# Kernel tuning notes

Measured on AMD Instinct MI355X. Metric: run time of the kernel, lower is better.

Reference implementation:

```python
import jax, jax.numpy as jnp
import numpy as np

HID, NQ, NKV, HD = 4096, 32, 8, 128
EPS = 1e-6
GOLDEN = 1.618033988749895
BASE = 10000.0


def _rmsnorm(x, w, eps=EPS):
    var = jnp.mean(x.astype(jnp.float32) ** 2, axis=-1, keepdims=True)
    return (x * jax.lax.rsqrt(var + eps)).astype(x.dtype) * w


def _rope_half(t, pos, inv_freq):
    # t: (B,T,H,dh); pos: (B,T); inv_freq: (dh//2,)
    ang = pos.astype(jnp.float32)[..., None] * inv_freq  # (B,T,dq)
    cos = jnp.cos(ang)[:, :, None, :]
    sin = jnp.sin(ang)[:, :, None, :]
    dq = inv_freq.shape[0]
    t1, t2 = t[..., :dq], t[..., dq:]
    return jnp.concatenate([t1 * cos - t2 * sin, t1 * sin + t2 * cos], axis=-1)


def _apply_ggrope(q, k, row_ids, col_ids):
    # 2D RoPE: first half of head_dim encodes rows, second half encodes cols;
    # column frequencies scaled by the golden ratio (GGRoPE).
    dh = HD // 2
    inv_freq = 1.0 / (BASE ** (jnp.arange(0, dh, 2, dtype=jnp.float32) / dh))
    inv_freq_col = inv_freq * GOLDEN

    def rot(t):
        tr = _rope_half(t[..., :dh], row_ids, inv_freq)
        tc = _rope_half(t[..., dh:], col_ids, inv_freq_col)
        return jnp.concatenate([tr, tc], axis=-1)

    return rot(q), rot(k)


def setup_inputs() -> dict:
    key = jax.random.key(0)
    ks = jax.random.split(key, 9)
    B, T = 1, 2048
    s = 0.02
    return {
        "x": jax.random.normal(ks[0], (B, T, HID), jnp.float32),
        "row_ids": jax.random.randint(ks[1], (B, T), 0, 30),
        "col_ids": jax.random.randint(ks[2], (B, T), 0, 30),
        "attention_mask": jnp.zeros((B, 1, T, T), jnp.float32),
        "Wq": jax.random.normal(ks[3], (HID, NQ * HD), jnp.float32) * s,
        "Wk": jax.random.normal(ks[4], (HID, NKV * HD), jnp.float32) * s,
        "Wv": jax.random.normal(ks[5], (HID, NKV * HD), jnp.float32) * s,
        "Wo": jax.random.normal(ks[6], (NQ * HD, HID), jnp.float32) * s,
        "q_norm_w": jnp.ones((HD,), jnp.float32),
        "k_norm_w": jnp.ones((HD,), jnp.float32),
    }


def reference(x, row_ids, col_ids, attention_mask, Wq, Wk, Wv, Wo, q_norm_w, k_norm_w):
    B, T, _ = x.shape
    group = NQ // NKV
    q = (x @ Wq).reshape(B, T, NQ, HD)
    k = (x @ Wk).reshape(B, T, NKV, HD)
    v = (x @ Wv).reshape(B, T, NKV, HD)
    q = _rmsnorm(q, q_norm_w)
    k = _rmsnorm(k, k_norm_w)
    q, k = _apply_ggrope(q, k, row_ids, col_ids)
    # expand KV heads to match query heads (GQA)
    k = jnp.repeat(k, group, axis=2)  # (B,T,NQ,HD)
    v = jnp.repeat(v, group, axis=2)
    q = q.transpose(0, 2, 1, 3)  # (B,NQ,T,HD)
    k = k.transpose(0, 2, 1, 3)
    v = v.transpose(0, 2, 1, 3)
    ssmax_scale = (HD ** -0.5) * np.log(max(T, 2)).astype(np.float32)
    scores = jnp.einsum("bhqd,bhkd->bhqk", q, k) * ssmax_scale
    scores = scores + attention_mask
    attn = jax.nn.softmax(scores.astype(jnp.float32), axis=-1).astype(q.dtype)
    out = jnp.einsum("bhqk,bhkd->bhqd", attn, v)
    out = out.transpose(0, 2, 1, 3).reshape(B, T, NQ * HD)
    return out @ Wo
```

## Files before the change

kernel.cpp:

```cpp
#include <hip/hip_runtime.h>
#include <hip/hip_bf16.h>

typedef unsigned short u16;
typedef __attribute__((ext_vector_type(8))) short bf16x8;
typedef __attribute__((ext_vector_type(4))) float f32x4;

#define LOG2E_F 1.4426950408889634f
#define QSCALE (0.08838834764831845f * 7.625595228825695f * 1.4426950408889634f)

__device__ __forceinline__ u16 f2bf(float f) {
  unsigned x = __float_as_uint(f);
  unsigned r = (x + 0x7fffu + ((x >> 16) & 1u)) >> 16;
  return (u16)r;
}
__device__ __forceinline__ float bf2f(u16 u) {
  return __uint_as_float(((unsigned)u) << 16);
}
__device__ __forceinline__ float exp2a(float x) {
  float r;
  asm("v_exp_f32 %0, %1" : "=v"(r) : "v"(x));
  return r;
}
__device__ __forceinline__ unsigned cvtpk(float lo, float hi) {
  unsigned r;
  asm("v_cvt_pk_bf16_f32 %0, %1, %2" : "=v"(r) : "v"(lo), "v"(hi));
  return r;
}

__device__ __forceinline__ void gload_lds16(const void* g, void* l) {
  __builtin_amdgcn_global_load_lds(
      (__attribute__((address_space(1))) void*)(g),
      (__attribute__((address_space(3))) void*)(l), 16, 0, 0);
}

__device__ __forceinline__ f32x4 mfma16(bf16x8 a, bf16x8 b, f32x4 c) {
  return __builtin_amdgcn_mfma_f32_16x16x32_bf16(a, b, c, 0, 0, 0);
}

__global__ __launch_bounds__(256) void cvt_x(const float4* __restrict__ x,
                                             ushort4* __restrict__ xb) {
  size_t i = (size_t)blockIdx.x * 256 + threadIdx.x;
  float4 v = x[i];
  ushort4 o;
  o.x = f2bf(v.x); o.y = f2bf(v.y); o.z = f2bf(v.z); o.w = f2bf(v.w);
  xb[i] = o;
}

__global__ __launch_bounds__(256) void tcvt(const float* __restrict__ src,
                                            u16* __restrict__ dst, int N) {
  __shared__ float t[64][65];
  int bid = blockIdx.x;
  int kt = bid & 63, nt = bid >> 6;
  int k0 = kt * 64, n0 = nt * 64;
  int tid = threadIdx.x;
#pragma unroll
  for (int it = 0; it < 16; ++it) {
    int idx = it * 256 + tid;
    int row = idx >> 6, col = idx & 63;
    t[row][col] = src[(size_t)(k0 + row) * N + n0 + col];
  }
  __syncthreads();
#pragma unroll
  for (int it = 0; it < 8; ++it) {
    int idx = it * 256 + tid;
    int nrow = idx >> 5, kc = idx & 31;
    ushort2 o;
    o.x = f2bf(t[kc * 2][nrow]);
    o.y = f2bf(t[kc * 2 + 1][nrow]);
    *(ushort2*)&dst[(size_t)(n0 + nrow) * 4096 + k0 + kc * 2] = o;
  }
}

__global__ __launch_bounds__(256) void maskflag(const float4* __restrict__ mask,
                                                int* __restrict__ flag) {
  size_t i = (size_t)blockIdx.x * 256 + threadIdx.x;
  float4 v = mask[i];
  if (v.x != 0.f || v.y != 0.f || v.z != 0.f || v.w != 0.f) atomicOr(flag, 1);
}

__global__ __launch_bounds__(256) void trig_kernel(const int* __restrict__ row_ids,
                                                   const int* __restrict__ col_ids,
                                                   float4* __restrict__ trig) {
  int idx = blockIdx.x * 256 + threadIdx.x;
  int tok = idx >> 5, i = idx & 31;
  float inv = exp2f(-(float)i * 0.41524101186092030f);
  float ar = (float)row_ids[tok] * inv;
  float ac = (float)col_ids[tok] * inv * 1.618033988749895f;
  float4 o;
  o.x = cosf(ar); o.y = sinf(ar); o.z = cosf(ac); o.w = sinf(ac);
  trig[idx] = o;
}

__global__ __launch_bounds__(256) void rope_kernel(u16* __restrict__ qk,
                                                   const float4* __restrict__ trig,
                                                   const float* __restrict__ qw,
                                                   const float* __restrict__ kw) {
  const int tok = blockIdx.x;
  const int tid = threadIdx.x;
  const int w = tid >> 6, lane = tid & 63;
  float4 t4 = trig[tok * 32 + (lane & 31)];
  float sgn = (lane < 32) ? -1.0f : 1.0f;

  for (int it = 0; it < 10; ++it) {
    int hh = w + it * 4;
    bool isQ = (hh < 32);
    int colbase = isQ ? hh * 128 : 4096 + (hh - 32) * 128;
    const float* nw = isQ ? qw : kw;
    float scale = isQ ? QSCALE : 1.0f;
    u16* p = qk + (size_t)tok * 5120 + colbase;
    float v1 = bf2f(p[lane]);
    float v2 = bf2f(p[64 + lane]);
    float w1 = nw[lane], w2 = nw[64 + lane];
    float ss = v1 * v1 + v2 * v2;
    ss += __shfl_xor(ss, 1);  ss += __shfl_xor(ss, 2);  ss += __shfl_xor(ss, 4);
    ss += __shfl_xor(ss, 8);  ss += __shfl_xor(ss, 16); ss += __shfl_xor(ss, 32);
    float rinv = rsqrtf(ss * (1.0f / 128.0f) + 1e-6f);
    float n1 = v1 * rinv * w1;
    float n2 = v2 * rinv * w2;
    float p1 = __shfl_xor(n1, 32);
    float p2 = __shfl_xor(n2, 32);
    float r1 = n1 * t4.x + sgn * p1 * t4.y;
    float r2 = n2 * t4.z + sgn * p2 * t4.w;
    p[lane]      = f2bf(r1 * scale);
    p[64 + lane] = f2bf(r2 * scale);
  }
}

template <int MODE>
__global__ __launch_bounds__(512, 2) void gemm256(const u16* __restrict__ A,
                                                  const u16* __restrict__ Bt,
                                                  void* __restrict__ C0,
                                                  u16* __restrict__ Vt, int nnt) {
  extern __shared__ char smem[];
  const int tid = threadIdx.x, lane = tid & 63, w = tid >> 6;
  const int l15 = lane & 15, l4 = lane >> 4;
  const int wr = w >> 2, wc = w & 3;

  const int grid = gridDim.x;
  const int wgid = (blockIdx.x & 7) * (grid >> 3) + (blockIdx.x >> 3);
  const int mt = wgid / nnt, nt = wgid % nnt;
  const int m0 = mt * 256, n0 = nt * 256;

  const int kswz = (((tid & 7) ^ ((tid >> 3) & 7)) << 4);
  const char* arow = (const char*)A + (size_t)(m0 + (tid >> 3)) * 8192 + kswz;
  const char* brow = (const char*)Bt + (size_t)(n0 + (tid >> 3)) * 8192 + kswz;

  auto stageA = [&](int t, int h) {
#pragma unroll
    for (int rd = 0; rd < 2; ++rd)
      gload_lds16(arow + (size_t)(h * 128 + rd * 64) * 8192 + t * 128,
                  smem + ((t & 1) * 2 + h) * 16384 + rd * 8192 + w * 1024);
  };
  auto stageB = [&](int t, int h) {
#pragma unroll
    for (int rd = 0; rd < 2; ++rd)
      gload_lds16(brow + (size_t)(h * 128 + rd * 64) * 8192 + t * 128,
                  smem + 65536 + ((t & 1) * 2 + h) * 16384 + rd * 8192 + w * 1024);
  };

  f32x4 acc[8][4];
#pragma unroll
  for (int i = 0; i < 8; ++i)
#pragma unroll
    for (int j = 0; j < 4; ++j) acc[i][j] = (f32x4){0.f, 0.f, 0.f, 0.f};

  const int aoff0 = ((l4) ^ (l15 & 7)) << 4;
  const int aoff1 = ((4 + l4) ^ (l15 & 7)) << 4;

  stageA(0, 0); stageA(0, 1);
  stageB(0, 0); stageB(0, 1);
  stageB(1, 0); stageB(1, 1);
  asm volatile("s_waitcnt vmcnt(4)" ::: "memory");
  __builtin_amdgcn_s_barrier();

  auto do_iter = [&](int t0, int last) {
    bf16x8 bfr[4][2];
#pragma unroll
    for (int p = 0; p < 8; ++p) {
      const int s = p >> 2, qd = p & 3;
      const char* aT = smem + (s * 2 + wr) * 16384 + l15 * 128;
      bf16x8 afr[2][2];
#pragma unroll
      for (int jm = 0; jm < 2; ++jm) {
        afr[jm][0] = *(const bf16x8*)(aT + (2 * qd + jm) * 2048 + aoff0);
        afr[jm][1] = *(const bf16x8*)(aT + (2 * qd + jm) * 2048 + aoff1);
      }
      if (qd == 0) {
        const char* bT = smem + 65536 + (s * 2 + (wc >> 1)) * 16384 +
                         ((wc & 1) * 64 + l15) * 128;
#pragma unroll
        for (int nf = 0; nf < 4; ++nf) {
          bfr[nf][0] = *(const bf16x8*)(bT + nf * 2048 + aoff0);
          bfr[nf][1] = *(const bf16x8*)(bT + nf * 2048 + aoff1);
        }
      }
      if (p == 0) { stageA(t0 + 1, 0); stageA(t0 + 1, 1); }
      if (!last) {
        if (p == 1) stageB(t0 + 2, 0);
        if (p == 2) stageB(t0 + 2, 1);
        if (p == 4) { stageA(t0 + 2, 0); stageA(t0 + 2, 1); }
        if (p == 5) stageB(t0 + 3, 0);
        if (p == 6) stageB(t0 + 3, 1);
      }
      if (p == 3) {
        if (last) asm volatile("s_waitcnt vmcnt(0)" ::: "memory");
        else      asm volatile("s_waitcnt vmcnt(4)" ::: "memory");
      }
      if (p == 7 && !last) asm volatile("s_waitcnt vmcnt(4)" ::: "memory");
      __builtin_amdgcn_s_barrier();
      asm volatile("s_waitcnt lgkmcnt(0)" ::: "memory");
      __builtin_amdgcn_sched_barrier(0);
      __builtin_amdgcn_s_setprio(1);
#pragma unroll
      for (int ks = 0; ks < 2; ++ks)
#pragma unroll
        for (int jm = 0; jm < 2; ++jm)
#pragma unroll
          for (int nf = 0; nf < 4; ++nf)
            acc[2 * qd + jm][nf] =
                mfma16(afr[jm][ks], bfr[nf][ks], acc[2 * qd + jm][nf]);
      __builtin_amdgcn_s_setprio(0);
      __builtin_amdgcn_s_barrier();
    }
  };

  for (int j = 0; j < 31; ++j) do_iter(2 * j, 0);
  do_iter(62, 1);

  if (MODE == 0) {
    if (n0 < 5120) {
      u16* qkp = (u16*)C0;
#pragma unroll
      for (int mf = 0; mf < 8; ++mf)
#pragma unroll
        for (int nf = 0; nf < 4; ++nf) {
          int ng = n0 + wc * 64 + nf * 16 + l15;
#pragma unroll
          for (int r = 0; r < 4; ++r) {
            int mg = m0 + wr * 128 + mf * 16 + l4 * 4 + r;
            qkp[(size_t)mg * 5120 + ng] = f2bf(acc[mf][nf][r]);
          }
        }
    } else {
#pragma unroll
      for (int mf = 0; mf < 8; ++mf)
#pragma unroll
        for (int nf = 0; nf < 4; ++nf) {
          int vr = (n0 - 5120) + wc * 64 + nf * 16 + l15;
          int mg = m0 + wr * 128 + mf * 16 + l4 * 4;
          ushort4 pk;
          pk.x = f2bf(acc[mf][nf][0]); pk.y = f2bf(acc[mf][nf][1]);
          pk.z = f2bf(acc[mf][nf][2]); pk.w = f2bf(acc[mf][nf][3]);
          *(ushort4*)&Vt[(size_t)vr * 2048 + mg] = pk;
        }
    }
  } else {
    float* Cp = (float*)C0;
#pragma unroll
    for (int mf = 0; mf < 8; ++mf)
#pragma unroll
      for (int nf = 0; nf < 4; ++nf) {
        int ng = n0 + wc * 64 + nf * 16 + l15;
#pragma unroll
        for (int r = 0; r < 4; ++r) {
          int mg = m0 + wr * 128 + mf * 16 + l4 * 4 + r;
          Cp[(size_t)mg * 4096 + ng] = acc[mf][nf][r];
        }
      }
  }
}

__global__ __launch_bounds__(512, 2) void attn_kernel(const u16* __restrict__ qk,
                                                      const u16* __restrict__ vt,
                                                      u16* __restrict__ oat,
                                                      const float* __restrict__ mask,
                                                      const int* __restrict__ flag) {
  __shared__ u16 k_lds[2][64 * 128];
  __shared__ u16 v_lds[2][64 * 128];

  const int tid = threadIdx.x, lane = tid & 63, w = tid >> 6;
  const int l15 = lane & 15, l4 = lane >> 4;
  const int bid = blockIdx.x;
  const int hk = bid & 7;
  const int rest = bid >> 3;
  const int h = hk * 4 + (rest & 3);
  const int qt = rest >> 2;
  const int qbase = qt * 256 + w * 32;

  const bool use_mask = (*flag != 0);
  const char* kbase = (const char*)qk + 8192 + (size_t)hk * 256;
  const char* vbase = (const char*)vt + (size_t)hk * 128 * 4096;

  bf16x8 qf[2][4];
#pragma unroll
  for (int qg = 0; qg < 2; ++qg) {
    const char* qp = (const char*)qk +
                     (size_t)(qbase + qg * 16 + l15) * 10240 + h * 256 + l4 * 16;
#pragma unroll
    for (int ks = 0; ks < 4; ++ks) qf[qg][ks] = *(const bf16x8*)(qp + ks * 64);
  }

  f32x4 oacc[2][8];
#pragma unroll
  for (int qg = 0; qg < 2; ++qg)
#pragma unroll
    for (int fd = 0; fd < 8; ++fd) oacc[qg][fd] = (f32x4){0.f, 0.f, 0.f, 0.f};
  float m_run[2] = {-1e30f, -1e30f};
  float l_run[2] = {0.f, 0.f};

  int koff[4], voff[2];
#pragma unroll
  for (int ks = 0; ks < 4; ++ks) koff[ks] = ((4 * ks + l4) ^ l15) << 4;
#pragma unroll
  for (int ks = 0; ks < 2; ++ks) voff[ks] = ((4 * ks + l4) ^ (l15 & 7)) << 4;

#define STAGE(buf, kv0)                                                        \
  {                                                                            \
    _Pragma("unroll") for (int rd = 0; rd < 2; ++rd) {                         \
      int c = rd * 512 + tid;                                                  \
      int row = c >> 4;                                                        \
      int src = ((c & 15) ^ (row & 15)) << 4;                                  \
      gload_lds16(kbase + (size_t)((kv0) + row) * 10240 + src,                 \
                  (char*)k_lds[buf] + (rd * 512 + w * 64) * 16);               \
      int rowv = c >> 3;                                                       \
      int srcv = ((c & 7) ^ (rowv & 7)) << 4;                                  \
      gload_lds16(vbase + (size_t)rowv * 4096 + (kv0) * 2 + srcv,              \
                  (char*)v_lds[buf] + (rd * 512 + w * 64) * 16);               \
    }                                                                          \
  }

  STAGE(0, 0);
  asm volatile("s_waitcnt vmcnt(0)" ::: "memory");
  __builtin_amdgcn_s_barrier();
  __builtin_amdgcn_sched_barrier(0);

  for (int kt = 0; kt < 32; ++kt) {
    const int cur = kt & 1;
    const int kv0 = kt * 64;
    if (kt < 31) STAGE(cur ^ 1, kv0 + 64);

    f32x4 sA[2][4];
#pragma unroll
    for (int qg = 0; qg < 2; ++qg)
#pragma unroll
      for (int f = 0; f < 4; ++f) sA[qg][f] = (f32x4){0.f, 0.f, 0.f, 0.f};

    __builtin_amdgcn_s_setprio(1);
#pragma unroll
    for (int ks = 0; ks < 4; ++ks) {
      bf16x8 kfr[4];
#pragma unroll
      for (int f = 0; f < 4; ++f)
        kfr[f] = *(const bf16x8*)((const char*)k_lds[cur] +
                                  (16 * f + l15) * 256 + koff[ks]);
#pragma unroll
      for (int f = 0; f < 4; ++f) {
        sA[0][f] = mfma16(kfr[f], qf[0][ks], sA[0][f]);
        sA[1][f] = mfma16(kfr[f], qf[1][ks], sA[1][f]);
      }
    }
    __builtin_amdgcn_s_setprio(0);

    if (use_mask) {
#pragma unroll
      for (int qg = 0; qg < 2; ++qg) {
        int qglob = qbase + qg * 16 + l15;
#pragma unroll
        for (int f = 0; f < 4; ++f)
#pragma unroll
          for (int r = 0; r < 4; ++r) {
            int kvglob = kv0 + 16 * f + 4 * l4 + r;
            sA[qg][f][r] += LOG2E_F * mask[(size_t)qglob * 2048 + kvglob];
          }
      }
    }

    unsigned paw[2][2][4];
#pragma unroll
    for (int qg = 0; qg < 2; ++qg) {
      float mx = fmaxf(fmaxf(fmaxf(sA[qg][0][0], sA[qg][0][1]),
                             fmaxf(sA[qg][0][2], sA[qg][0][3])),
                       fmaxf(fmaxf(sA[qg][1][0], sA[qg][1][1]),
                             fmaxf(sA[qg][1][2], sA[qg][1][3])));
      float mx2 = fmaxf(fmaxf(fmaxf(sA[qg][2][0], sA[qg][2][1]),
                              fmaxf(sA[qg][2][2], sA[qg][2][3])),
                        fmaxf(fmaxf(sA[qg][3][0], sA[qg][3][1]),
                              fmaxf(sA[qg][3][2], sA[qg][3][3])));
      mx = fmaxf(mx, mx2);
      mx = fmaxf(mx, __shfl_xor(mx, 16));
      mx = fmaxf(mx, __shfl_xor(mx, 32));
      if (__any(mx > m_run[qg] + 8.0f)) {
        float mnew = fmaxf(m_run[qg], mx);
        float a = exp2a(m_run[qg] - mnew);
        l_run[qg] *= a;
        m_run[qg] = mnew;
        float a0 = __shfl(a, 4 * l4 + 0);
        float a1 = __shfl(a, 4 * l4 + 1);
        float a2 = __shfl(a, 4 * l4 + 2);
        float a3 = __shfl(a, 4 * l4 + 3);
#pragma unroll
        for (int fd = 0; fd < 8; ++fd) {
          oacc[qg][fd][0] *= a0; oacc[qg][fd][1] *= a1;
          oacc[qg][fd][2] *= a2; oacc[qg][fd][3] *= a3;
        }
      }
      float ps = 0.f;
      unsigned W[4][2];
#pragma unroll
      for (int f = 0; f < 4; ++f) {
        float p0 = exp2a(sA[qg][f][0] - m_run[qg]);
        float p1 = exp2a(sA[qg][f][1] - m_run[qg]);
        float p2 = exp2a(sA[qg][f][2] - m_run[qg]);
        float p3 = exp2a(sA[qg][f][3] - m_run[qg]);
        ps += (p0 + p1) + (p2 + p3);
        W[f][0] = cvtpk(p0, p1);
        W[f][1] = cvtpk(p2, p3);
      }
      ps += __shfl_xor(ps, 16);
      ps += __shfl_xor(ps, 32);
      l_run[qg] += ps;
#pragma unroll
      for (int ks = 0; ks < 2; ++ks)
#pragma unroll
        for (int wd = 0; wd < 4; ++wd) {
          int src = l15 + 16 * (2 * (l4 & 1) + (wd >> 1));
          unsigned v0 = (unsigned)__shfl((int)W[2 * ks][wd & 1], src);
          unsigned v1 = (unsigned)__shfl((int)W[2 * ks + 1][wd & 1], src);
          paw[qg][ks][wd] = (l4 & 2) ? v1 : v0;
        }
    }

    __builtin_amdgcn_s_setprio(1);
#pragma unroll
    for (int ks = 0; ks < 2; ++ks) {
      union { unsigned u[4]; bf16x8 v; } pa0, pa1;
#pragma unroll
      for (int wd = 0; wd < 4; ++wd) {
        pa0.u[wd] = paw[0][ks][wd];
        pa1.u[wd] = paw[1][ks][wd];
      }
#pragma unroll
      for (int fd = 0; fd < 8; ++fd) {
        bf16x8 vb = *(const bf16x8*)((const char*)v_lds[cur] +
                                     (16 * fd + l15) * 128 + voff[ks]);
        oacc[0][fd] = mfma16(pa0.v, vb, oacc[0][fd]);
        oacc[1][fd] = mfma16(pa1.v, vb, oacc[1][fd]);
      }
    }
    __builtin_amdgcn_s_setprio(0);

    if (kt < 31) {
      asm volatile("s_waitcnt vmcnt(0)" ::: "memory");
      __builtin_amdgcn_s_barrier();
      __builtin_amdgcn_sched_barrier(0);
    }
  }

#pragma unroll
  for (int qg = 0; qg < 2; ++qg) {
    float inv[4];
#pragma unroll
    for (int r = 0; r < 4; ++r) inv[r] = 1.0f / __shfl(l_run[qg], 4 * l4 + r);
#pragma unroll
    for (int fd = 0; fd < 8; ++fd) {
      int dg = h * 128 + 16 * fd + l15;
#pragma unroll
      for (int r = 0; r < 4; ++r) {
        int qrow = qbase + qg * 16 + 4 * l4 + r;
        oat[(size_t)qrow * 4096 + dg] = f2bf(oacc[qg][fd][r] * inv[r]);
      }
    }
  }
#undef STAGE
}

extern "C" void kernel_launch(void* const* d_in, const int* in_sizes, int n_in,
                              void* d_out, int out_size, void* d_ws, size_t ws_size,
                              hipStream_t stream) {
  const float* x = (const float*)d_in[0];
  const int* row_ids = (const int*)d_in[1];
  const int* col_ids = (const int*)d_in[2];
  const float* mask = (const float*)d_in[3];
  const float* Wq = (const float*)d_in[4];
  const float* Wk = (const float*)d_in[5];
  const float* Wv = (const float*)d_in[6];
  const float* Wo = (const float*)d_in[7];
  const float* qw = (const float*)d_in[8];
  const float* kw = (const float*)d_in[9];

  char* ws = (char*)d_ws;
  u16* xb      = (u16*)(ws);
  u16* wqkvt   = (u16*)(ws + 16777216);
  u16* wot     = (u16*)(ws + 67108864);
  u16* qkbuf   = (u16*)(ws + 100663296);
  u16* vtbuf   = (u16*)(ws + 121634816);
  u16* oat     = (u16*)(ws + 125829120);
  float4* trig = (float4*)(ws + 142606336);
  int* flag    = (int*)(ws + 143654912);

  hipFuncSetAttribute((const void*)gemm256<0>,
                      hipFuncAttributeMaxDynamicSharedMemorySize, 131072);
  hipFuncSetAttribute((const void*)gemm256<1>,
                      hipFuncAttributeMaxDynamicSharedMemorySize, 131072);

  hipMemsetAsync(flag, 0, 4, stream);
  maskflag<<<4096, 256, 0, stream>>>((const float4*)mask, flag);
  cvt_x<<<8192, 256, 0, stream>>>((const float4*)x, (ushort4*)xb);
  tcvt<<<64 * 64, 256, 0, stream>>>(Wq, wqkvt, 4096);
  tcvt<<<64 * 16, 256, 0, stream>>>(Wk, wqkvt + (size_t)4096 * 4096, 1024);
  tcvt<<<64 * 16, 256, 0, stream>>>(Wv, wqkvt + (size_t)5120 * 4096, 1024);
  tcvt<<<64 * 64, 256, 0, stream>>>(Wo, wot, 4096);
  trig_kernel<<<256, 256, 0, stream>>>(row_ids, col_ids, trig);
  gemm256<0><<<192, 512, 131072, stream>>>(xb, wqkvt, (void*)qkbuf, vtbuf, 24);
  rope_kernel<<<2048, 256, 0, stream>>>(qkbuf, trig, qw, kw);
  attn_kernel<<<256, 512, 0, stream>>>(qkbuf, vtbuf, oat, mask, flag);
  gemm256<1><<<128, 512, 131072, stream>>>(oat, wot, d_out, nullptr, 16);
}
```

Measured before the change: 385.1 us.

## Retile QKV GEMM to 256x192 tiles and split-K the output projection

The QKV projection GEMM now uses 256x192 tiles, giving 256 workgroups instead of 192 so the grid maps more evenly onto the device's compute units. A single B stage of three rows replaces the two-half B staging, and the wait counts are adjusted to match. The output projection is split along K into two halves, giving 256 workgroups that write fp32 partial results to workspace, and a new reduce kernel adds the two halves. The cost is extra partial-sum memory traffic, one more kernel launch, and reuse of the start of the workspace (which also holds the bf16 copy of x) as the partial buffer.

After: 365.1 us. 1.05x faster.

```diff
diff --git a/kernel.cpp b/kernel.cpp
--- a/kernel.cpp
+++ b/kernel.cpp
@@ -135,11 +135,16 @@
   const int tid = threadIdx.x, lane = tid & 63, w = tid >> 6;
   const int l15 = lane & 15, l4 = lane >> 4;
   const int wr = w >> 2, wc = w & 3;
-
-  const int grid = gridDim.x;
-  const int wgid = (blockIdx.x & 7) * (grid >> 3) + (blockIdx.x >> 3);
+  constexpr int NF = (MODE == 0) ? 3 : 4;
+  constexpr int BNW = (MODE == 0) ? 48 : 64;
+
+  int wgid = (blockIdx.x & 7) * (gridDim.x >> 3) + (blockIdx.x >> 3);
+  int kh = 0;
+  if (MODE == 1) { kh = wgid >> 7; wgid &= 127; }
   const int mt = wgid / nnt, nt = wgid % nnt;
-  const int m0 = mt * 256, n0 = nt * 256;
+  const int m0 = mt * 256;
+  const int n0 = nt * ((MODE == 0) ? 192 : 256);
+  const int tbase = kh * 32;
 
   const int kswz = (((tid & 7) ^ ((tid >> 3) & 7)) << 4);
   const char* arow = (const char*)A + (size_t)(m0 + (tid >> 3)) * 8192 + kswz;
@@ -151,30 +156,41 @@
       gload_lds16(arow + (size_t)(h * 128 + rd * 64) * 8192 + t * 128,
                   smem + ((t & 1) * 2 + h) * 16384 + rd * 8192 + w * 1024);
   };
-  auto stageB = [&](int t, int h) {
+  auto stageB0 = [&](int t) {
+#pragma unroll
+    for (int rd = 0; rd < 3; ++rd)
+      gload_lds16(brow + (size_t)(rd * 64) * 8192 + t * 128,
+                  smem + 65536 + (t & 1) * 24576 + rd * 8192 + w * 1024);
+  };
+  auto stageB1 = [&](int t, int h) {
 #pragma unroll
     for (int rd = 0; rd < 2; ++rd)
       gload_lds16(brow + (size_t)(h * 128 + rd * 64) * 8192 + t * 128,
                   smem + 65536 + ((t & 1) * 2 + h) * 16384 + rd * 8192 + w * 1024);
   };
 
-  f32x4 acc[8][4];
+  f32x4 acc[8][NF];
 #pragma unroll
   for (int i = 0; i < 8; ++i)
 #pragma unroll
-    for (int j = 0; j < 4; ++j) acc[i][j] = (f32x4){0.f, 0.f, 0.f, 0.f};
+    for (int j = 0; j < NF; ++j) acc[i][j] = (f32x4){0.f, 0.f, 0.f, 0.f};
 
   const int aoff0 = ((l4) ^ (l15 & 7)) << 4;
   const int aoff1 = ((4 + l4) ^ (l15 & 7)) << 4;
 
-  stageA(0, 0); stageA(0, 1);
-  stageB(0, 0); stageB(0, 1);
-  stageB(1, 0); stageB(1, 1);
-  asm volatile("s_waitcnt vmcnt(4)" ::: "memory");
+  stageA(tbase, 0); stageA(tbase, 1);
+  if constexpr (MODE == 0) {
+    stageB0(tbase); stageB0(tbase + 1);
+    asm volatile("s_waitcnt vmcnt(3)" ::: "memory");
+  } else {
+    stageB1(tbase, 0); stageB1(tbase, 1);
+    stageB1(tbase + 1, 0); stageB1(tbase + 1, 1);
+    asm volatile("s_waitcnt vmcnt(4)" ::: "memory");
+  }
   __builtin_amdgcn_s_barrier();
 
   auto do_iter = [&](int t0, int last) {
-    bf16x8 bfr[4][2];
+    bf16x8 bfr[NF][2];
 #pragma unroll
     for (int p = 0; p < 8; ++p) {
       const int s = p >> 2, qd = p & 3;
@@ -186,27 +202,44 @@
         afr[jm][1] = *(const bf16x8*)(aT + (2 * qd + jm) * 2048 + aoff1);
       }
       if (qd == 0) {
-        const char* bT = smem + 65536 + (s * 2 + (wc >> 1)) * 16384 +
-                         ((wc & 1) * 64 + l15) * 128;
-#pragma unroll
-        for (int nf = 0; nf < 4; ++nf) {
+        const char* bT;
+        if constexpr (MODE == 0)
+          bT = smem + 65536 + s * 24576 + (wc * 48 + l15) * 128;
+        else
+          bT = smem + 65536 + (s * 2 + (wc >> 1)) * 16384 +
+               ((wc & 1) * 64 + l15) * 128;
+#pragma unroll
+        for (int nf = 0; nf < NF; ++nf) {
           bfr[nf][0] = *(const bf16x8*)(bT + nf * 2048 + aoff0);
           bfr[nf][1] = *(const bf16x8*)(bT + nf * 2048 + aoff1);
         }
       }
       if (p == 0) { stageA(t0 + 1, 0); stageA(t0 + 1, 1); }
       if (!last) {
-        if (p == 1) stageB(t0 + 2, 0);
-        if (p == 2) stageB(t0 + 2, 1);
+        if constexpr (MODE == 0) {
+          if (p == 1) stageB0(t0 + 2);
+          if (p == 5) stageB0(t0 + 3);
+        } else {
+          if (p == 1) stageB1(t0 + 2, 0);
+          if (p == 2) stageB1(t0 + 2, 1);
+          if (p == 5) stageB1(t0 + 3, 0);
+          if (p == 6) stageB1(t0 + 3, 1);
+        }
         if (p == 4) { stageA(t0 + 2, 0); stageA(t0 + 2, 1); }
-        if (p == 5) stageB(t0 + 3, 0);
-        if (p == 6) stageB(t0 + 3, 1);
       }
       if (p == 3) {
         if (last) asm volatile("s_waitcnt vmcnt(0)" ::: "memory");
-        else      asm volatile("s_waitcnt vmcnt(4)" ::: "memory");
-      }
-      if (p == 7 && !last) asm volatile("s_waitcnt vmcnt(4)" ::: "memory");
+        else if constexpr (MODE == 0)
+          asm volatile("s_waitcnt vmcnt(3)" ::: "memory");
+        else
+          asm volatile("s_waitcnt vmcnt(4)" ::: "memory");
+      }
+      if (p == 7 && !last) {
+        if constexpr (MODE == 0)
+          asm volatile("s_waitcnt vmcnt(3)" ::: "memory");
+        else
+          asm volatile("s_waitcnt vmcnt(4)" ::: "memory");
+      }
       __builtin_amdgcn_s_barrier();
       asm volatile("s_waitcnt lgkmcnt(0)" ::: "memory");
       __builtin_amdgcn_sched_barrier(0);
@@ -216,7 +249,7 @@
 #pragma unroll
         for (int jm = 0; jm < 2; ++jm)
 #pragma unroll
-          for (int nf = 0; nf < 4; ++nf)
+          for (int nf = 0; nf < NF; ++nf)
             acc[2 * qd + jm][nf] =
                 mfma16(afr[jm][ks], bfr[nf][ks], acc[2 * qd + jm][nf]);
       __builtin_amdgcn_s_setprio(0);
@@ -224,43 +257,39 @@
     }
   };
 
-  for (int j = 0; j < 31; ++j) do_iter(2 * j, 0);
-  do_iter(62, 1);
+  constexpr int NIT = (MODE == 0) ? 32 : 16;
+  for (int j = 0; j < NIT - 1; ++j) do_iter(tbase + 2 * j, 0);
+  do_iter(tbase + 2 * (NIT - 1), 1);
 
   if (MODE == 0) {
-    if (n0 < 5120) {
-      u16* qkp = (u16*)C0;
-#pragma unroll
-      for (int mf = 0; mf < 8; ++mf)
-#pragma unroll
-        for (int nf = 0; nf < 4; ++nf) {
-          int ng = n0 + wc * 64 + nf * 16 + l15;
+    u16* qkp = (u16*)C0;
+#pragma unroll
+    for (int mf = 0; mf < 8; ++mf)
+#pragma unroll
+      for (int nf = 0; nf < NF; ++nf) {
+        int ng = n0 + wc * BNW + nf * 16 + l15;
+        if (ng < 5120) {
 #pragma unroll
           for (int r = 0; r < 4; ++r) {
             int mg = m0 + wr * 128 + mf * 16 + l4 * 4 + r;
             qkp[(size_t)mg * 5120 + ng] = f2bf(acc[mf][nf][r]);
           }
-        }
-    } else {
-#pragma unroll
-      for (int mf = 0; mf < 8; ++mf)
-#pragma unroll
-        for (int nf = 0; nf < 4; ++nf) {
-          int vr = (n0 - 5120) + wc * 64 + nf * 16 + l15;
+        } else {
+          int vr = ng - 5120;
           int mg = m0 + wr * 128 + mf * 16 + l4 * 4;
           ushort4 pk;
           pk.x = f2bf(acc[mf][nf][0]); pk.y = f2bf(acc[mf][nf][1]);
           pk.z = f2bf(acc[mf][nf][2]); pk.w = f2bf(acc[mf][nf][3]);
           *(ushort4*)&Vt[(size_t)vr * 2048 + mg] = pk;
         }
-    }
+      }
   } else {
-    float* Cp = (float*)C0;
+    float* Cp = (float*)C0 + (size_t)kh * 8388608;
 #pragma unroll
     for (int mf = 0; mf < 8; ++mf)
 #pragma unroll
-      for (int nf = 0; nf < 4; ++nf) {
-        int ng = n0 + wc * 64 + nf * 16 + l15;
+      for (int nf = 0; nf < NF; ++nf) {
+        int ng = n0 + wc * BNW + nf * 16 + l15;
 #pragma unroll
         for (int r = 0; r < 4; ++r) {
           int mg = m0 + wr * 128 + mf * 16 + l4 * 4 + r;
@@ -268,6 +297,16 @@
         }
       }
   }
+}
+
+__global__ __launch_bounds__(256) void reduce2(const float4* __restrict__ p0,
+                                               const float4* __restrict__ p1,
+                                               float4* __restrict__ out) {
+  size_t i = (size_t)blockIdx.x * 256 + threadIdx.x;
+  float4 a = p0[i], b = p1[i];
+  float4 o;
+  o.x = a.x + b.x; o.y = a.y + b.y; o.z = a.z + b.z; o.w = a.w + b.w;
+  out[i] = o;
 }
 
 __global__ __launch_bounds__(512, 2) void attn_kernel(const u16* __restrict__ qk,
@@ -497,6 +536,7 @@
   u16* oat     = (u16*)(ws + 125829120);
   float4* trig = (float4*)(ws + 142606336);
   int* flag    = (int*)(ws + 143654912);
+  float* pbuf  = (float*)(ws);
 
   hipFuncSetAttribute((const void*)gemm256<0>,
                       hipFuncAttributeMaxDynamicSharedMemorySize, 131072);
@@ -511,8 +551,11 @@
   tcvt<<<64 * 16, 256, 0, stream>>>(Wv, wqkvt + (size_t)5120 * 4096, 1024);
   tcvt<<<64 * 64, 256, 0, stream>>>(Wo, wot, 4096);
   trig_kernel<<<256, 256, 0, stream>>>(row_ids, col_ids, trig);
-  gemm256<0><<<192, 512, 131072, stream>>>(xb, wqkvt, (void*)qkbuf, vtbuf, 24);
+  gemm256<0><<<256, 512, 114688, stream>>>(xb, wqkvt, (void*)qkbuf, vtbuf, 32);
   rope_kernel<<<2048, 256, 0, stream>>>(qkbuf, trig, qw, kw);
   attn_kernel<<<256, 512, 0, stream>>>(qkbuf, vtbuf, oat, mask, flag);
-  gemm256<1><<<128, 512, 131072, stream>>>(oat, wot, d_out, nullptr, 16);
-}
+  gemm256<1><<<256, 512, 131072, stream>>>(oat, wot, (void*)pbuf, nullptr, 16);
+  reduce2<<<8192, 256, 0, stream>>>((const float4*)pbuf,
+                                    (const float4*)(pbuf + 8388608),
+                                    (float4*)d_out);
+}
```
